# Optimization experiments

Measured on AMD Instinct MI355X. Metric: run time of the kernel, lower is better.

## Reference

```python
import jax, jax.numpy as jnp
import numpy as np


def setup_inputs() -> dict:
    key = jax.random.key(0)
    x = jax.random.normal(key, (4, 512, 64, 64), dtype=jnp.float32)
    return {"x": x}


def reference(x) -> jnp.ndarray:
    B, C, H, W = x.shape
    N = H * W
    v = x.reshape(B, C, N)                      # proj_query/key/value all = x flattened
    # energy[b, i, j] = sum_c x[b,c,i] * x[b,c,j]
    energy = jnp.einsum('bci,bcj->bij', v, v)
    attention = jax.nn.softmax(energy, axis=-1)  # softmax over last dim (keys j)
    # out[b,c,i] = sum_j v[b,c,j] * attention[b,i,j]  (== V @ attention^T)
    out = jnp.einsum('bcj,bij->bci', v, attention)
    return out.reshape(B, C, H, W)
```

## Files before the change

kernel.cpp:

```cpp
#include <hip/hip_runtime.h>
#include <hip/hip_bf16.h>

typedef unsigned short u16;
typedef unsigned int   u32;
typedef unsigned long long u64;
typedef __attribute__((ext_vector_type(8))) short bf16x8;
typedef __attribute__((ext_vector_type(4))) float f32x4;

#define BB 4
#define CC 512
#define NN 4096
#define LOG2E 1.44269504f

static __device__ __forceinline__ u16 f2b(float f) {
    __hip_bfloat16 h = __float2bfloat16(f);
    return *(u16*)&h;
}
static __device__ __forceinline__ u16 f2b_fast(float f) {
    u32 u = __builtin_bit_cast(u32, f);
    return (u16)((u + 0x8000u) >> 16);
}
static __device__ __forceinline__ float b2f(u16 b) {
    u32 u = (u32)b << 16;
    return __builtin_bit_cast(float, u);
}

typedef __attribute__((address_space(1))) const u32 GU32;
typedef __attribute__((address_space(3))) u32 LU32;
__device__ __forceinline__ void async16(const void* g, void* l) {
    __builtin_amdgcn_global_load_lds((GU32*)g, (LU32*)l, 16, 0, 0);
}

__global__ __launch_bounds__(256) void prep_kernel(const float* __restrict__ x,
                                                   u16* __restrict__ XT,
                                                   u16* __restrict__ XN,
                                                   float* __restrict__ norms) {
    __shared__ __align__(8) u16 tile[64][68];
    __shared__ float nsum[64];
    int blk = blockIdx.x;
    int b  = blk >> 9;
    int r2 = blk & 511;
    int c0 = (r2 >> 6) << 6;
    int n0 = (r2 & 63) << 6;
    int t  = threadIdx.x;
    if (t < 64) nsum[t] = 0.f;

    int nq    = t & 15;
    int rbase = t >> 4;
    float psum[4] = {0.f, 0.f, 0.f, 0.f};
    #pragma unroll
    for (int p = 0; p < 4; ++p) {
        int cl = p * 16 + rbase;
        const float* src = x + ((size_t)(b * CC + c0 + cl) * NN) + n0 + nq * 4;
        float4 v = *(const float4*)src;
        psum[0] += v.x * v.x; psum[1] += v.y * v.y;
        psum[2] += v.z * v.z; psum[3] += v.w * v.w;
        u64 pk = (u64)f2b(v.x) | ((u64)f2b(v.y) << 16) |
                 ((u64)f2b(v.z) << 32) | ((u64)f2b(v.w) << 48);
        *(u64*)&XN[((size_t)(b * CC + c0 + cl) * NN) + n0 + nq * 4] = pk;
        *(u64*)&tile[cl][nq * 4] = pk;
    }
    __syncthreads();
    int c2 = (t & 31) * 2;
    int nb = t >> 5;
    #pragma unroll
    for (int rr = 0; rr < 8; ++rr) {
        int nl = rr * 8 + nb;
        u32 lo = tile[c2][nl], hi = tile[c2 + 1][nl];
        *(u32*)&XT[((size_t)(b * NN + n0 + nl) * CC) + c0 + c2] = lo | (hi << 16);
    }
    #pragma unroll
    for (int k = 0; k < 4; ++k) atomicAdd(&nsum[nq * 4 + k], psum[k]);
    __syncthreads();
    if (t < 64) atomicAdd(&norms[(size_t)b * NN + n0 + t], nsum[t]);
}

__global__ __launch_bounds__(256) void maxn_kernel(const float* __restrict__ norms,
                                                   float* __restrict__ maxn) {
    int b = blockIdx.x, t = threadIdx.x;
    float m = 0.f;
    for (int k = t; k < NN; k += 256) m = fmaxf(m, norms[(size_t)b * NN + k]);
    #pragma unroll
    for (int d = 1; d < 64; d <<= 1) m = fmaxf(m, __shfl_xor(m, d));
    __shared__ float wred[4];
    if ((t & 63) == 0) wred[t >> 6] = m;
    __syncthreads();
    if (t == 0) maxn[b] = fmaxf(fmaxf(wred[0], wred[1]), fmaxf(wred[2], wred[3]));
}

__global__ __launch_bounds__(256, 2) void flash_kernel(const u16* __restrict__ XT,
                                                       const u16* __restrict__ XN,
                                                       const float* __restrict__ norms,
                                                       const float* __restrict__ maxn,
                                                       float* __restrict__ outF,
                                                       u16* __restrict__ outH,
                                                       float* __restrict__ l0g,
                                                       float* __restrict__ l1g,
                                                       int split) {
    __shared__ __align__(16) u16 KtT[2][32 * 520];
    __shared__ __align__(16) u16 Plds[2][64 * 40];
    __shared__ float lLds[64];

    int blk   = blockIdx.x;
    int inner = blk & 255;
    int hf    = split ? (blk >> 8) : 0;
    int xcd = inner & 7;
    int b   = xcd >> 1;
    int ib  = (inner >> 3) + ((xcd & 1) << 5);
    int i_base = ib * 64;
    int jlo = hf * (NN / 2) * split;
    int njt = split ? 64 : 128;

    int t    = threadIdx.x;
    int w    = t >> 6;
    int lane = t & 63;
    int l15  = lane & 15;
    int q    = lane >> 4;

    const u16* xtb = XT + (size_t)b * NN * CC;
    const u16* xnb = XN + (size_t)b * CC * NN;

    float mxn = maxn[b];
    float M2[4];
    #pragma unroll
    for (int r = 0; r < 4; ++r) {
        float nr = norms[(size_t)b * NN + i_base + w * 16 + q * 4 + r];
        M2[r] = (sqrtf(nr * mxn) - 40.f) * LOG2E;
    }

    bf16x8 qf[16];
    {
        const u16* qrow = xtb + (size_t)(i_base + w * 16 + l15) * CC;
        #pragma unroll
        for (int kk = 0; kk < 16; ++kk)
            qf[kk] = *(const bf16x8*)(qrow + kk * 32 + q * 8);
    }

    f32x4 o[8][4];
    #pragma unroll
    for (int ct = 0; ct < 8; ++ct)
        #pragma unroll
        for (int it = 0; it < 4; ++it)
            o[ct][it] = (f32x4){0.f, 0.f, 0.f, 0.f};
    float lpart[4] = {0.f, 0.f, 0.f, 0.f};

    {
        const u16* src = xtb + (size_t)(jlo + w * 8) * CC + lane * 8;
        #pragma unroll
        for (int rr = 0; rr < 8; ++rr)
            async16(src + rr * CC, &KtT[0][(w * 8 + rr) * 520]);
    }
    __syncthreads();

    for (int jt = 0; jt < njt; ++jt) {
        int buf = jt & 1;
        int j0  = jlo + jt * 32;

        bf16x8 vf[8];
        #pragma unroll
        for (int ct = 0; ct < 8; ++ct)
            vf[ct] = *(const bf16x8*)(xnb + (size_t)(w * 128 + ct * 16 + l15) * NN + j0 + q * 8);

        if (jt + 1 < njt) {
            const u16* src = xtb + (size_t)(j0 + 32 + w * 8) * CC + lane * 8;
            #pragma unroll
            for (int rr = 0; rr < 8; ++rr)
                async16(src + rr * CC, &KtT[buf ^ 1][(w * 8 + rr) * 520]);
        }

        f32x4 s0 = {0.f,0.f,0.f,0.f}, s1 = {0.f,0.f,0.f,0.f};
        #pragma unroll
        for (int kk = 0; kk < 16; ++kk) {
            bf16x8 b0 = *(const bf16x8*)&KtT[buf][(l15)      * 520 + kk * 32 + q * 8];
            bf16x8 b1 = *(const bf16x8*)&KtT[buf][(16 + l15) * 520 + kk * 32 + q * 8];
            s0 = __builtin_amdgcn_mfma_f32_16x16x32_bf16(qf[kk], b0, s0, 0, 0, 0);
            s1 = __builtin_amdgcn_mfma_f32_16x16x32_bf16(qf[kk], b1, s1, 0, 0, 0);
        }

        #pragma unroll
        for (int r = 0; r < 4; ++r) {
            float p0 = __builtin_amdgcn_exp2f(fmaf(s0[r], LOG2E, -M2[r]));
            float p1 = __builtin_amdgcn_exp2f(fmaf(s1[r], LOG2E, -M2[r]));
            u16 h0 = f2b_fast(p0), h1 = f2b_fast(p1);
            lpart[r] += b2f(h0) + b2f(h1);
            int row = w * 16 + q * 4 + r;
            Plds[buf][row * 40 +      l15] = h0;
            Plds[buf][row * 40 + 16 + l15] = h1;
        }
        __syncthreads();

        bf16x8 pb[4];
        #pragma unroll
        for (int it = 0; it < 4; ++it)
            pb[it] = *(const bf16x8*)&Plds[buf][(it * 16 + l15) * 40 + q * 8];
        #pragma unroll
        for (int ct = 0; ct < 8; ++ct)
            #pragma unroll
            for (int it = 0; it < 4; ++it)
                o[ct][it] = __builtin_amdgcn_mfma_f32_16x16x32_bf16(vf[ct], pb[it], o[ct][it], 0, 0, 0);
    }

    #pragma unroll
    for (int r = 0; r < 4; ++r) {
        float s = lpart[r];
        s += __shfl_xor(s, 1);
        s += __shfl_xor(s, 2);
        s += __shfl_xor(s, 4);
        s += __shfl_xor(s, 8);
        lpart[r] = s;
    }

    if (!split) {
        if (l15 == 0) {
            #pragma unroll
            for (int r = 0; r < 4; ++r) lLds[w * 16 + q * 4 + r] = lpart[r];
        }
        __syncthreads();
        float linv[4];
        #pragma unroll
        for (int it = 0; it < 4; ++it) linv[it] = 1.f / lLds[it * 16 + l15];
        float* ob = outF + (size_t)b * CC * NN;
        #pragma unroll
        for (int ct = 0; ct < 8; ++ct)
            #pragma unroll
            for (int r = 0; r < 4; ++r) {
                int c = w * 128 + ct * 16 + q * 4 + r;
                float* orow = ob + (size_t)c * NN + i_base;
                #pragma unroll
                for (int it = 0; it < 4; ++it)
                    orow[it * 16 + l15] = o[ct][it][r] * linv[it];
            }
    } else {
        if (l15 == 0) {
            float* lg = (hf == 0) ? l0g : l1g;
            #pragma unroll
            for (int r = 0; r < 4; ++r)
                lg[(size_t)b * NN + i_base + w * 16 + q * 4 + r] = lpart[r];
        }
        if (hf == 0) {
            float* ob = outF + (size_t)b * CC * NN;
            #pragma unroll
            for (int ct = 0; ct < 8; ++ct)
                #pragma unroll
                for (int r = 0; r < 4; ++r) {
                    int c = w * 128 + ct * 16 + q * 4 + r;
                    float* orow = ob + (size_t)c * NN + i_base;
                    #pragma unroll
                    for (int it = 0; it < 4; ++it)
                        orow[it * 16 + l15] = o[ct][it][r];
                }
        } else {
            u16* ob = outH + (size_t)b * CC * NN;
            #pragma unroll
            for (int ct = 0; ct < 8; ++ct)
                #pragma unroll
                for (int r = 0; r < 4; ++r) {
                    int c = w * 128 + ct * 16 + q * 4 + r;
                    u16* orow = ob + (size_t)c * NN + i_base;
                    #pragma unroll
                    for (int it = 0; it < 4; ++it)
                        orow[it * 16 + l15] = f2b(o[ct][it][r]);
                }
        }
    }
}

__global__ __launch_bounds__(256) void combine_kernel(float* __restrict__ out,
                                                      const u16* __restrict__ P1,
                                                      const float* __restrict__ l0,
                                                      const float* __restrict__ l1) {
    size_t g = (size_t)blockIdx.x * 256 + threadIdx.x;
    size_t f = g * 4;
    int i = (int)(f & (NN - 1));
    int b = (int)(f >> 21);
    float4 p0 = *(float4*)&out[f];
    u64 pk = *(const u64*)&P1[f];
    float p0a[4] = {p0.x, p0.y, p0.z, p0.w};
    float r[4];
    #pragma unroll
    for (int k = 0; k < 4; ++k) {
        float l = l0[(size_t)b * NN + i + k] + l1[(size_t)b * NN + i + k];
        float p1f = b2f((u16)((pk >> (16 * k)) & 0xFFFFu));
        r[k] = (p0a[k] + p1f) / l;
    }
    *(float4*)&out[f] = (float4){r[0], r[1], r[2], r[3]};
}

extern "C" void kernel_launch(void* const* d_in, const int* in_sizes, int n_in,
                              void* d_out, int out_size, void* d_ws, size_t ws_size,
                              hipStream_t stream) {
    const float* x = (const float*)d_in[0];
    size_t SZ = (size_t)BB * NN * CC;
    u16* XT = (u16*)d_ws;
    u16* XN = XT + SZ;
    u16* P1 = XN + SZ;
    float* norms = (float*)(P1 + SZ);
    float* l0g   = norms + (size_t)BB * NN;
    float* l1g   = l0g + (size_t)BB * NN;
    float* maxn  = l1g + (size_t)BB * NN;
    size_t needed = 3 * SZ * 2 + 3 * (size_t)BB * NN * 4 + 64;
    int split = (ws_size >= needed) ? 1 : 0;
    float* out = (float*)d_out;
    if (!split) {
        norms = (float*)(XN + SZ);
        l0g = norms + (size_t)BB * NN;
        l1g = l0g;
        maxn = l1g + (size_t)BB * NN;
    }

    hipMemsetAsync(norms, 0, (size_t)BB * NN * sizeof(float), stream);
    prep_kernel<<<2048, 256, 0, stream>>>(x, XT, XN, norms);
    maxn_kernel<<<BB, 256, 0, stream>>>(norms, maxn);
    if (split) {
        flash_kernel<<<512, 256, 0, stream>>>(XT, XN, norms, maxn, out, P1, l0g, l1g, 1);
        combine_kernel<<<(BB * CC * NN / 4) / 256, 256, 0, stream>>>(out, P1, l0g, l1g);
    } else {
        flash_kernel<<<256, 256, 0, stream>>>(XT, XN, norms, maxn, out, P1, l0g, l1g, 0);
    }
}
```

Before: 294.7 us.

## Fuse norm max reduction into prep kernel and strength-reduce flash loop addressing

The prep kernel now loops over all 512 channels per 64-column block, so each block owns its norms outright. It writes them directly instead of atomically accumulating, and it folds the per-batch max into an integer atomicMax on the float bits. This removes the norms memset and the separate maxn kernel launch. In the flash kernel, per-iteration address arithmetic is replaced with incrementing pointers. The trade-off is that prep drops from 2048 to 256 blocks, which lowers parallelism for a bandwidth-bound transpose/convert pass.

```diff
diff --git a/kernel.cpp b/kernel.cpp
--- a/kernel.cpp
+++ b/kernel.cpp
@@ -34,64 +34,61 @@
 __global__ __launch_bounds__(256) void prep_kernel(const float* __restrict__ x,
                                                    u16* __restrict__ XT,
                                                    u16* __restrict__ XN,
-                                                   float* __restrict__ norms) {
+                                                   float* __restrict__ norms,
+                                                   int* __restrict__ maxn) {
     __shared__ __align__(8) u16 tile[64][68];
     __shared__ float nsum[64];
     int blk = blockIdx.x;
-    int b  = blk >> 9;
-    int r2 = blk & 511;
-    int c0 = (r2 >> 6) << 6;
-    int n0 = (r2 & 63) << 6;
+    int b  = blk >> 6;
+    int n0 = (blk & 63) << 6;
     int t  = threadIdx.x;
     if (t < 64) nsum[t] = 0.f;
 
     int nq    = t & 15;
     int rbase = t >> 4;
     float psum[4] = {0.f, 0.f, 0.f, 0.f};
-    #pragma unroll
-    for (int p = 0; p < 4; ++p) {
-        int cl = p * 16 + rbase;
-        const float* src = x + ((size_t)(b * CC + c0 + cl) * NN) + n0 + nq * 4;
-        float4 v = *(const float4*)src;
-        psum[0] += v.x * v.x; psum[1] += v.y * v.y;
-        psum[2] += v.z * v.z; psum[3] += v.w * v.w;
-        u64 pk = (u64)f2b(v.x) | ((u64)f2b(v.y) << 16) |
-                 ((u64)f2b(v.z) << 32) | ((u64)f2b(v.w) << 48);
-        *(u64*)&XN[((size_t)(b * CC + c0 + cl) * NN) + n0 + nq * 4] = pk;
-        *(u64*)&tile[cl][nq * 4] = pk;
-    }
-    __syncthreads();
-    int c2 = (t & 31) * 2;
-    int nb = t >> 5;
-    #pragma unroll
-    for (int rr = 0; rr < 8; ++rr) {
-        int nl = rr * 8 + nb;
-        u32 lo = tile[c2][nl], hi = tile[c2 + 1][nl];
-        *(u32*)&XT[((size_t)(b * NN + n0 + nl) * CC) + c0 + c2] = lo | (hi << 16);
+
+    for (int c0 = 0; c0 < CC; c0 += 64) {
+        #pragma unroll
+        for (int p = 0; p < 4; ++p) {
+            int cl = p * 16 + rbase;
+            const float* src = x + ((size_t)(b * CC + c0 + cl) * NN) + n0 + nq * 4;
+            float4 v = *(const float4*)src;
+            psum[0] += v.x * v.x; psum[1] += v.y * v.y;
+            psum[2] += v.z * v.z; psum[3] += v.w * v.w;
+            u64 pk = (u64)f2b(v.x) | ((u64)f2b(v.y) << 16) |
+                     ((u64)f2b(v.z) << 32) | ((u64)f2b(v.w) << 48);
+            *(u64*)&XN[((size_t)(b * CC + c0 + cl) * NN) + n0 + nq * 4] = pk;
+            *(u64*)&tile[cl][nq * 4] = pk;
+        }
+        __syncthreads();
+        int c2 = (t & 31) * 2;
+        int nb = t >> 5;
+        #pragma unroll
+        for (int rr = 0; rr < 8; ++rr) {
+            int nl = rr * 8 + nb;
+            u32 val = (u32)tile[c2][nl] | ((u32)tile[c2 + 1][nl] << 16);
+            *(u32*)&XT[((size_t)(b * NN + n0 + nl) * CC) + c0 + c2] = val;
+        }
+        __syncthreads();
     }
     #pragma unroll
     for (int k = 0; k < 4; ++k) atomicAdd(&nsum[nq * 4 + k], psum[k]);
     __syncthreads();
-    if (t < 64) atomicAdd(&norms[(size_t)b * NN + n0 + t], nsum[t]);
-}
-
-__global__ __launch_bounds__(256) void maxn_kernel(const float* __restrict__ norms,
-                                                   float* __restrict__ maxn) {
-    int b = blockIdx.x, t = threadIdx.x;
-    float m = 0.f;
-    for (int k = t; k < NN; k += 256) m = fmaxf(m, norms[(size_t)b * NN + k]);
-    #pragma unroll
-    for (int d = 1; d < 64; d <<= 1) m = fmaxf(m, __shfl_xor(m, d));
-    __shared__ float wred[4];
-    if ((t & 63) == 0) wred[t >> 6] = m;
-    __syncthreads();
-    if (t == 0) maxn[b] = fmaxf(fmaxf(wred[0], wred[1]), fmaxf(wred[2], wred[3]));
+    if (t < 64) {
+        float v = nsum[t];
+        norms[(size_t)b * NN + n0 + t] = v;
+        float m = v;
+        #pragma unroll
+        for (int d = 1; d < 64; d <<= 1) m = fmaxf(m, __shfl_xor(m, d));
+        if (t == 0) atomicMax(&maxn[b], __float_as_int(m));
+    }
 }
 
 __global__ __launch_bounds__(256, 2) void flash_kernel(const u16* __restrict__ XT,
                                                        const u16* __restrict__ XN,
                                                        const float* __restrict__ norms,
-                                                       const float* __restrict__ maxn,
+                                                       const int* __restrict__ maxn,
                                                        float* __restrict__ outF,
                                                        u16* __restrict__ outH,
                                                        float* __restrict__ l0g,
@@ -120,7 +117,7 @@
     const u16* xtb = XT + (size_t)b * NN * CC;
     const u16* xnb = XN + (size_t)b * CC * NN;
 
-    float mxn = maxn[b];
+    float mxn = __int_as_float(maxn[b]);
     float M2[4];
     #pragma unroll
     for (int r = 0; r < 4; ++r) {
@@ -144,6 +141,9 @@
             o[ct][it] = (f32x4){0.f, 0.f, 0.f, 0.f};
     float lpart[4] = {0.f, 0.f, 0.f, 0.f};
 
+    const u16* vfp = xnb + (size_t)(w * 128 + l15) * NN + jlo + q * 8;
+    const u16* stp = xtb + (size_t)(jlo + 32 + w * 8) * CC + lane * 8;
+
     {
         const u16* src = xtb + (size_t)(jlo + w * 8) * CC + lane * 8;
         #pragma unroll
@@ -154,19 +154,19 @@
 
     for (int jt = 0; jt < njt; ++jt) {
         int buf = jt & 1;
-        int j0  = jlo + jt * 32;
 
         bf16x8 vf[8];
         #pragma unroll
         for (int ct = 0; ct < 8; ++ct)
-            vf[ct] = *(const bf16x8*)(xnb + (size_t)(w * 128 + ct * 16 + l15) * NN + j0 + q * 8);
+            vf[ct] = *(const bf16x8*)(vfp + (size_t)ct * 16 * NN);
+        vfp += 32;
 
         if (jt + 1 < njt) {
-            const u16* src = xtb + (size_t)(j0 + 32 + w * 8) * CC + lane * 8;
             #pragma unroll
             for (int rr = 0; rr < 8; ++rr)
-                async16(src + rr * CC, &KtT[buf ^ 1][(w * 8 + rr) * 520]);
-        }
+                async16(stp + rr * CC, &KtT[buf ^ 1][(w * 8 + rr) * 520]);
+        }
+        stp += 32 * CC;
 
         f32x4 s0 = {0.f,0.f,0.f,0.f}, s1 = {0.f,0.f,0.f,0.f};
         #pragma unroll
@@ -297,7 +297,7 @@
     float* norms = (float*)(P1 + SZ);
     float* l0g   = norms + (size_t)BB * NN;
     float* l1g   = l0g + (size_t)BB * NN;
-    float* maxn  = l1g + (size_t)BB * NN;
+    int*   maxn  = (int*)(l1g + (size_t)BB * NN);
     size_t needed = 3 * SZ * 2 + 3 * (size_t)BB * NN * 4 + 64;
     int split = (ws_size >= needed) ? 1 : 0;
     float* out = (float*)d_out;
@@ -305,12 +305,11 @@
         norms = (float*)(XN + SZ);
         l0g = norms + (size_t)BB * NN;
         l1g = l0g;
-        maxn = l1g + (size_t)BB * NN;
-    }
-
-    hipMemsetAsync(norms, 0, (size_t)BB * NN * sizeof(float), stream);
-    prep_kernel<<<2048, 256, 0, stream>>>(x, XT, XN, norms);
-    maxn_kernel<<<BB, 256, 0, stream>>>(norms, maxn);
+        maxn = (int*)(l1g + (size_t)BB * NN);
+    }
+
+    hipMemsetAsync(maxn, 0, BB * sizeof(int), stream);
+    prep_kernel<<<256, 256, 0, stream>>>(x, XT, XN, norms, maxn);
     if (split) {
         flash_kernel<<<512, 256, 0, stream>>>(XT, XN, norms, maxn, out, P1, l0g, l1g, 1);
         combine_kernel<<<(BB * CC * NN / 4) / 256, 256, 0, stream>>>(out, P1, l0g, l1g);
```

Result: slower. 363.4 us (+23.3%).
